# Performance work log

Hardware: AMD Instinct MI355X
Metric: run time of the kernel (lower is better)

## Reference

```python
import jax, jax.numpy as jnp
import numpy as np

B, S, HID = 2, 2048, 1024
NH, NKV = 16, 4
HD = HID // NH          # 64
NREP = NH // NKV        # 4
EPS = 1e-06


def _rotate_half(x):
    h = x.shape[-1] // 2
    return jnp.concatenate([-x[..., h:], x[..., :h]], axis=-1)


def _rope(q, k, cos, sin):
    # q: [b,s,h,d], k: [b,s,kv,d]; cos/sin: [s,d] -> unsqueeze head dim
    c = cos[:, None, :]
    s = sin[:, None, :]
    return q * c + _rotate_half(q) * s, k * c + _rotate_half(k) * s


def setup_inputs() -> dict:
    key = jax.random.key(0)
    ks = jax.random.split(key, 8)
    sc = 0.02
    return {
        "x": jax.random.normal(ks[0], (B, S, HID), jnp.float32),
        "cos": jnp.cos(jnp.arange(S, dtype=jnp.float32)[:, None] *
                       (1.0 / (1e6 ** (jnp.arange(HD, dtype=jnp.float32) / HD)))),
        "sin": jnp.sin(jnp.arange(S, dtype=jnp.float32)[:, None] *
                       (1.0 / (1e6 ** (jnp.arange(HD, dtype=jnp.float32) / HD)))),
        "attention_mask": jnp.ones((B, S), jnp.int32),
        "Wq": jax.random.normal(ks[1], (HID, NH * HD), jnp.float32) * sc,
        "Wk": jax.random.normal(ks[2], (HID, NKV * HD), jnp.float32) * sc,
        "Wv": jax.random.normal(ks[3], (HID, NKV * HD), jnp.float32) * sc,
        "Wo": jax.random.normal(ks[4], (NH * HD, HID), jnp.float32) * sc,
    }


def reference(x, cos, sin, attention_mask, Wq, Wk, Wv, Wo):
    b, s, _ = x.shape
    q = (x @ Wq).reshape(b, s, NH, HD)
    k = (x @ Wk).reshape(b, s, NKV, HD)
    v = (x @ Wv).reshape(b, s, NKV, HD)
    q, k = _rope(q, k, cos[:s], sin[:s])
    # GQA repeat: [b,s,kv,d] -> [b,s,h,d]
    k = jnp.repeat(k, NREP, axis=2)
    v = jnp.repeat(v, NREP, axis=2)
    # -> [b,h,s,d]
    q = jnp.transpose(q, (0, 2, 1, 3))
    k = jnp.transpose(k, (0, 2, 1, 3))
    v = jnp.transpose(v, (0, 2, 1, 3))
    # feature map: elu(x) + 1 (positive features)
    q = jax.nn.elu(q) + 1.0
    k = jax.nn.elu(k) + 1.0
    # prefill path (seq_len > 1): non-causal kernelized scores
    scores = jnp.einsum("bhsd,bhtd->bhst", q, k)  # [b,h,s,s]
    mask = attention_mask[:, None, None, :]       # [b,1,1,s]
    scores = jnp.where(mask == 0, 0.0, scores)
    denom = jnp.clip(
        jax.lax.stop_gradient(jnp.abs(scores).sum(-1, keepdims=True)), 1e-06, None)
    scores = scores / denom
    out = jnp.einsum("bhst,bhtd->bhsd", scores, v)
    out = jnp.transpose(out, (0, 2, 1, 3)).reshape(b, s, NH * HD)
    return out @ Wo
```

## Files before the change

### kernel.cpp

```cpp
#include <hip/hip_runtime.h>
#include <hip/hip_bf16.h>

using u16 = unsigned short;
using u32 = unsigned int;

namespace {
constexpr int S   = 2048;
constexpr int HID = 1024;
constexpr int M   = 4096;
constexpr int K   = 1024;
}

typedef __attribute__((ext_vector_type(8))) short short8;
typedef __attribute__((ext_vector_type(4))) float f32x4;

__device__ __forceinline__ u16 f2bf(float f) {
    u32 u = __builtin_bit_cast(u32, f);
    u += 0x7fffu + ((u >> 16) & 1u);
    return (u16)(u >> 16);
}
__device__ __forceinline__ float bf2f(u16 h) {
    return __builtin_bit_cast(float, (u32)h << 16);
}
__device__ __forceinline__ float phi(float x) {
    return x > 0.f ? x + 1.f : __expf(x);
}
__device__ __forceinline__ void glds16(const u16* g, u16* l) {
    __builtin_amdgcn_global_load_lds(
        (const __attribute__((address_space(1))) u32*)g,
        (__attribute__((address_space(3))) u32*)l, 16, 0, 0);
}

template <int MODE>
__global__ __launch_bounds__(256, 3) void gemm_k(
    const u16* __restrict__ A, const u16* __restrict__ B,
    u16* __restrict__ Cq, float* __restrict__ Ckv,
    float* __restrict__ Cf, int ldc, int zAr, int zBr, int zCr,
    const float* __restrict__ Cos, const float* __restrict__ Sin,
    const int* __restrict__ Mask)
{
    constexpr int BK = 64;
    constexpr int NT = K / BK;
    __shared__ __align__(16) u16 sA0[64 * BK],  sA1[64 * BK];
    __shared__ __align__(16) u16 sB0[128 * BK], sB1[128 * BK];

    A += (size_t)blockIdx.z * zAr * K;
    B += (size_t)blockIdx.z * zBr * K;
    if (MODE == 1) Cf += (size_t)blockIdx.z * zCr * ldc;

    const int tid  = threadIdx.x;
    const int lane = tid & 63, w = tid >> 6;
    const int wm = w & 1, wn = w >> 1;
    const int m0 = blockIdx.x * 64, n0 = blockIdx.y * 128;
    const int fr = lane & 15, fq = lane >> 4;

    const int srow  = lane >> 3;
    const int sslot = lane & 7;
    const int sswz  = (sslot ^ srow) * 8;

    const u16* Asrc = A + (size_t)(m0 + w * 8 + srow) * K + sswz;
    const u16* Bsrc = B + (size_t)(n0 + w * 8 + srow) * K + sswz;
    const int ldsb = (w * 8) * BK;

    f32x4 acc[2][4] = {};

#define STAGE(dA, dB, kt)                                          \
    do {                                                           \
        glds16(Asrc + (kt),                 dA + ldsb);            \
        glds16(Asrc + (size_t)32 * K + (kt), dA + 32 * BK + ldsb); \
        glds16(Bsrc + (kt),                 dB + ldsb);            \
        glds16(Bsrc + (size_t)32 * K + (kt), dB + 32 * BK + ldsb); \
        glds16(Bsrc + (size_t)64 * K + (kt), dB + 64 * BK + ldsb); \
        glds16(Bsrc + (size_t)96 * K + (kt), dB + 96 * BK + ldsb); \
    } while (0)

#define COMPUTE(sAc, sBc)                                                    \
    do {                                                                     \
        _Pragma("unroll")                                                    \
        for (int kk = 0; kk < 2; ++kk) {                                     \
            const int ks = ((kk * 4 + fq) ^ (fr & 7)) * 8;                   \
            short8 ah[2], bh[4];                                             \
            _Pragma("unroll")                                                \
            for (int i = 0; i < 2; ++i)                                      \
                ah[i] = *(const short8*)(sAc + (wm * 32 + i * 16 + fr) * BK + ks); \
            _Pragma("unroll")                                                \
            for (int j = 0; j < 4; ++j)                                      \
                bh[j] = *(const short8*)(sBc + (wn * 64 + j * 16 + fr) * BK + ks); \
            _Pragma("unroll")                                                \
            for (int i = 0; i < 2; ++i)                                      \
                _Pragma("unroll")                                            \
                for (int j = 0; j < 4; ++j)                                  \
                    acc[i][j] = __builtin_amdgcn_mfma_f32_16x16x32_bf16(     \
                        ah[i], bh[j], acc[i][j], 0, 0, 0);                   \
        }                                                                    \
    } while (0)

#define SYNC()                                              \
    do {                                                    \
        asm volatile("s_waitcnt vmcnt(0)" ::: "memory");    \
        __syncthreads();                                    \
    } while (0)

    STAGE(sA0, sB0, 0);
    SYNC();
#pragma unroll 1
    for (int t = 0; t < NT; t += 2) {
        if (t + 1 < NT) STAGE(sA1, sB1, (t + 1) * BK);
        COMPUTE(sA0, sB0);
        SYNC();
        if (t + 2 < NT) STAGE(sA0, sB0, (t + 2) * BK);
        COMPUTE(sA1, sB1);
        SYNC();
    }
#undef STAGE
#undef COMPUTE
#undef SYNC

    const bool isQ = (MODE == 0) && (n0 < 1024);
    const bool isK = (MODE == 0) && (n0 >= 1024) && (n0 < 1280);
#pragma unroll
    for (int i = 0; i < 2; ++i)
#pragma unroll
        for (int jj = 0; jj < 4; ++jj) {
            const int row = m0 + wm * 32 + i * 16 + fq * 4 + jj;
            float v0 = acc[i][0][jj], v1 = acc[i][1][jj];
            float v2 = acc[i][2][jj], v3 = acc[i][3][jj];
            if (MODE == 1) {
                float* cr = &Cf[(size_t)row * ldc + n0 + wn * 64 + fr];
                cr[0] = v0; cr[16] = v1; cr[32] = v2; cr[48] = v3;
                continue;
            }
            if (isQ || isK) {
                const int sb = (row & (S - 1)) * 64;
                float r0 = v0 * Cos[sb + fr]      - v2 * Sin[sb + fr];
                float r2 = v2 * Cos[sb + fr + 32] + v0 * Sin[sb + fr + 32];
                float r1 = v1 * Cos[sb + fr + 16] - v3 * Sin[sb + fr + 16];
                float r3 = v3 * Cos[sb + fr + 48] + v1 * Sin[sb + fr + 48];
                v0 = phi(r0); v1 = phi(r1); v2 = phi(r2); v3 = phi(r3);
            }
            if (isQ) {
                u16* cr = &Cq[(size_t)row * 1024 + n0 + wn * 64 + fr];
                cr[0]  = f2bf(v0); cr[16] = f2bf(v1);
                cr[32] = f2bf(v2); cr[48] = f2bf(v3);
            } else if (isK) {
                const float mv = (float)Mask[row];
                float* cr = &Ckv[(size_t)row * 512 + (n0 - 1024) + wn * 64 + fr];
                cr[0] = v0 * mv; cr[16] = v1 * mv;
                cr[32] = v2 * mv; cr[48] = v3 * mv;
            } else {
                float* cr = &Ckv[(size_t)row * 512 + 256 + (n0 - 1280) + wn * 64 + fr];
                cr[0] = v0; cr[16] = v1; cr[32] = v2; cr[48] = v3;
            }
        }
}

__global__ __launch_bounds__(256) void prep_k(
    const float* __restrict__ X,  u16* __restrict__ Xb,
    const float* __restrict__ Wq, const float* __restrict__ Wk,
    const float* __restrict__ Wv, const float* __restrict__ Wo,
    u16* __restrict__ wt, u16* __restrict__ wot)
{
    const int bid = blockIdx.x, tid = threadIdx.x;
    if (bid < 4096) {
        const int i = (bid * 256 + tid) * 4;
        float4 v = *reinterpret_cast<const float4*>(&X[i]);
        ushort4 h;
        h.x = f2bf(v.x); h.y = f2bf(v.y); h.z = f2bf(v.z); h.w = f2bf(v.w);
        *reinterpret_cast<ushort4*>(&Xb[i]) = h;
        return;
    }
    int r = bid - 4096;
    const float* W; u16* T; int N, nbase, bx, by;
    if (r < 1024)      { W = Wq; T = wt;  N = 1024; nbase = 0;    bx = r & 31; by = r >> 5; }
    else if (r < 1280) { r -= 1024; W = Wk; T = wt; N = 256; nbase = 1024; bx = r & 7; by = r >> 3; }
    else if (r < 1536) { r -= 1280; W = Wv; T = wt; N = 256; nbase = 1280; bx = r & 7; by = r >> 3; }
    else               { r -= 1536; W = Wo; T = wot; N = 1024; nbase = 0;  bx = r & 31; by = r >> 5; }

    __shared__ float t[32][33];
    const int n0 = bx * 32, k0 = by * 32;
    const int tx = tid & 31, ty = tid >> 5;
#pragma unroll
    for (int i = 0; i < 4; ++i)
        t[ty + i * 8][tx] = W[(size_t)(k0 + ty + i * 8) * N + n0 + tx];
    __syncthreads();
#pragma unroll
    for (int i = 0; i < 4; ++i) {
        const int n = ty + i * 8;
        T[(size_t)(nbase + n0 + n) * 1024 + k0 + tx] = f2bf(t[tx][n]);
    }
}

__global__ __launch_bounds__(256) void kv_stage1_k(
    const float* __restrict__ KVf, float* __restrict__ part)
{
    const int g  = blockIdx.x;
    const int ch = blockIdx.y;
    const int b  = g >> 2, kvh = g & 3;
    const int tid = threadIdx.x;

    __shared__ float ks[64][64];
    __shared__ float vs[64][64];
    const int m0 = b * S + ch * 64;
#pragma unroll
    for (int l = 0; l < 4; ++l) {
        int idx = tid + l * 256;
        int r = idx >> 4, q4 = (idx & 15) * 4;
        const float* src = KVf + (size_t)(m0 + r) * 512 + kvh * 64;
        *reinterpret_cast<float4*>(&ks[r][q4]) = *reinterpret_cast<const float4*>(src + q4);
        *reinterpret_cast<float4*>(&vs[r][q4]) = *reinterpret_cast<const float4*>(src + 256 + q4);
    }
    __syncthreads();

    const int i = tid >> 2, j0 = (tid & 3) * 16;
    float4 a0 = {0,0,0,0}, a1 = {0,0,0,0}, a2 = {0,0,0,0}, a3 = {0,0,0,0};
#pragma unroll 8
    for (int r = 0; r < 64; ++r) {
        float kv = ks[r][i];
        float4 w0 = *reinterpret_cast<const float4*>(&vs[r][j0]);
        float4 w1 = *reinterpret_cast<const float4*>(&vs[r][j0 + 4]);
        float4 w2 = *reinterpret_cast<const float4*>(&vs[r][j0 + 8]);
        float4 w3 = *reinterpret_cast<const float4*>(&vs[r][j0 + 12]);
        a0.x = fmaf(kv, w0.x, a0.x); a0.y = fmaf(kv, w0.y, a0.y);
        a0.z = fmaf(kv, w0.z, a0.z); a0.w = fmaf(kv, w0.w, a0.w);
        a1.x = fmaf(kv, w1.x, a1.x); a1.y = fmaf(kv, w1.y, a1.y);
        a1.z = fmaf(kv, w1.z, a1.z); a1.w = fmaf(kv, w1.w, a1.w);
        a2.x = fmaf(kv, w2.x, a2.x); a2.y = fmaf(kv, w2.y, a2.y);
        a2.z = fmaf(kv, w2.z, a2.z); a2.w = fmaf(kv, w2.w, a2.w);
        a3.x = fmaf(kv, w3.x, a3.x); a3.y = fmaf(kv, w3.y, a3.y);
        a3.z = fmaf(kv, w3.z, a3.z); a3.w = fmaf(kv, w3.w, a3.w);
    }
    float* dst = part + ((size_t)g * 32 + ch) * 4160;
    float* d0 = dst + i * 64 + j0;
    *reinterpret_cast<float4*>(d0)      = a0;
    *reinterpret_cast<float4*>(d0 + 4)  = a1;
    *reinterpret_cast<float4*>(d0 + 8)  = a2;
    *reinterpret_cast<float4*>(d0 + 12) = a3;
    if (tid < 64) {
        float ksum = 0.f;
#pragma unroll 8
        for (int r = 0; r < 64; ++r) ksum += ks[r][tid];
        dst[4096 + tid] = ksum;
    }
}

__global__ __launch_bounds__(256) void kv_reduce_k(
    const float* __restrict__ part, u16* __restrict__ KVh,
    float* __restrict__ Ksumf)
{
    const int g = blockIdx.x;
    const int e = blockIdx.y * 256 + threadIdx.x;
    if (e >= 4160) return;
    const float* p = part + (size_t)g * 32 * 4160 + e;
    float s = 0.f;
#pragma unroll 8
    for (int c = 0; c < 32; ++c) s += p[(size_t)c * 4160];
    if (e < 4096) KVh[g * 4096 + e] = f2bf(s);
    else          Ksumf[g * 64 + (e - 4096)] = s;
}

__global__ __launch_bounds__(256, 2) void kw_gemm_k(
    const u16* __restrict__ WoT, const u16* __restrict__ KVb,
    u16* __restrict__ KWT)
{
    __shared__ __align__(16) u16 sA[128 * 64];
    __shared__ __align__(16) u16 sB[64 * 64];

    const int tid = threadIdx.x, lane = tid & 63, w = tid >> 6;
    const int o0 = blockIdx.x * 128;
    const int gh = blockIdx.y, b = gh >> 4, h = gh & 15, g = b * 4 + (h >> 2);
    const int fr = lane & 15, fq = lane >> 4;
    const int srow = lane >> 3, sslot = lane & 7;
    const int sswz = (sslot ^ srow) * 8;

#pragma unroll
    for (int c = 0; c < 4; ++c) {
        const int rb = w * 32 + c * 8;
        glds16(WoT + (size_t)(o0 + rb + srow) * 1024 + h * 64 + sswz, sA + rb * 64);
    }
#pragma unroll
    for (int c = 0; c < 2; ++c) {
        const int rb = w * 16 + c * 8;
        glds16(KVb + (size_t)g * 4096 + (rb + srow) * 64 + sswz, sB + rb * 64);
    }
    asm volatile("s_waitcnt vmcnt(0)" ::: "memory");
    __syncthreads();

    f32x4 acc[2][4] = {};
#pragma unroll
    for (int kk = 0; kk < 2; ++kk) {
        short8 a_h[2], b_h[4];
#pragma unroll
        for (int i = 0; i < 2; ++i) {
            const int row = w * 32 + i * 16 + fr;
            a_h[i] = *(const short8*)(sA + row * 64 + ((kk * 4 + fq) ^ (fr & 7)) * 8);
        }
#pragma unroll
        for (int j = 0; j < 4; ++j) {
            const int row = j * 16 + fr;
            b_h[j] = *(const short8*)(sB + row * 64 + ((kk * 4 + fq) ^ (fr & 7)) * 8);
        }
#pragma unroll
        for (int i = 0; i < 2; ++i)
#pragma unroll
            for (int j = 0; j < 4; ++j)
                acc[i][j] = __builtin_amdgcn_mfma_f32_16x16x32_bf16(
                    a_h[i], b_h[j], acc[i][j], 0, 0, 0);
    }
#pragma unroll
    for (int i = 0; i < 2; ++i)
#pragma unroll
        for (int j = 0; j < 4; ++j)
#pragma unroll
            for (int jj = 0; jj < 4; ++jj) {
                const int row = o0 + w * 32 + i * 16 + fq * 4 + jj;
                const int col = j * 16 + fr;
                KWT[((size_t)b * 1024 + row) * 1024 + h * 64 + col] =
                    f2bf(acc[i][j][jj]);
            }
}

__global__ __launch_bounds__(256) void qhat_k(
    const u16* __restrict__ Qt, const float* __restrict__ Ksumf,
    u16* __restrict__ Qh)
{
    const int t = blockIdx.x * 256 + threadIdx.x;
    const int m = t >> 4, h = t & 15;
    const int g = (m >> 11) * 4 + (h >> 2);
    const u16* q  = Qt + (size_t)m * 1024 + h * 64;
    const float* Ks = Ksumf + g * 64;

    float qv[64];
    float den = 0.f;
#pragma unroll
    for (int c = 0; c < 8; ++c) {
        short8 v8 = *reinterpret_cast<const short8*>(q + c * 8);
#pragma unroll
        for (int j = 0; j < 8; ++j) {
            qv[c * 8 + j] = bf2f((u16)v8[j]);
            den = fmaf(qv[c * 8 + j], Ks[c * 8 + j], den);
        }
    }
    const float rd = 1.f / fmaxf(den, 1e-6f);
    u16* o = Qh + (size_t)m * 1024 + h * 64;
#pragma unroll
    for (int c = 0; c < 8; ++c) {
        short8 ov;
#pragma unroll
        for (int j = 0; j < 8; ++j) ov[j] = (short)f2bf(qv[c * 8 + j] * rd);
        *reinterpret_cast<short8*>(o + c * 8) = ov;
    }
}

extern "C" void kernel_launch(void* const* d_in, const int* in_sizes, int n_in,
                              void* d_out, int out_size, void* d_ws, size_t ws_size,
                              hipStream_t stream)
{
    const float* x    = (const float*)d_in[0];
    const float* cosp = (const float*)d_in[1];
    const float* sinp = (const float*)d_in[2];
    const int*   msk  = (const int*)d_in[3];
    const float* Wq   = (const float*)d_in[4];
    const float* Wk   = (const float*)d_in[5];
    const float* Wv   = (const float*)d_in[6];
    const float* Wo   = (const float*)d_in[7];
    float* out = (float*)d_out;

    u16* xbf  = (u16*)d_ws;
    u16* wt   = xbf  + (size_t)M * K;
    u16* wot  = wt   + (size_t)1536 * K;
    u16* qt   = wot  + (size_t)K * K;
    u16* qhat = qt   + (size_t)M * K;
    u16* kvb  = qhat + (size_t)M * K;
    u16* kwt  = kvb  + 8 * 4096;
    float* kvf   = (float*)(kwt + (size_t)2 * K * K);
    float* part  = kvf + (size_t)M * 512;
    float* ksumf = part + (size_t)8 * 32 * 4160;

    prep_k<<<4096 + 1024 + 256 + 256 + 1024, 256, 0, stream>>>(
        x, xbf, Wq, Wk, Wv, Wo, wt, wot);

    gemm_k<0><<<dim3(M / 64, 1536 / 128, 1), 256, 0, stream>>>(
        xbf, wt, qt, kvf, nullptr, 0, 0, 0, 0, cosp, sinp, msk);

    kv_stage1_k<<<dim3(8, 32), 256, 0, stream>>>(kvf, part);
    kv_reduce_k<<<dim3(8, 17), 256, 0, stream>>>(part, kvb, ksumf);

    kw_gemm_k<<<dim3(8, 32), 256, 0, stream>>>(wot, kvb, kwt);

    qhat_k<<<(M * 16) / 256, 256, 0, stream>>>(qt, ksumf, qhat);

    gemm_k<1><<<dim3(2048 / 64, HID / 128, 2), 256, 0, stream>>>(
        qhat, kwt, nullptr, nullptr, out, HID, 2048, 1024, 2048,
        nullptr, nullptr, nullptr);
}
```

Baseline: 70.14 us.

## Deepen GEMM prefetch pipeline and merge KW gemm with qhat kernel

The GEMM main loop now issues two stages of global-to-LDS loads up front and waits with partial vmcnt counts and raw barriers, so the next tile's loads overlap the current compute instead of draining fully each step. Separately, the KW GEMM and the qhat normalization kernels are merged into one launch, with block index selecting the role, removing a launch and letting both run concurrently. The partial vmcnt count assumes an exact number of outstanding loads per stage, which is fragile. The merged kernel also loses the occupancy hint of 2 in its launch bounds.

```diff
diff --git a/kernel.cpp b/kernel.cpp
--- a/kernel.cpp
+++ b/kernel.cpp
@@ -95,26 +95,27 @@
         }                                                                    \
     } while (0)
 
-#define SYNC()                                              \
-    do {                                                    \
-        asm volatile("s_waitcnt vmcnt(0)" ::: "memory");    \
-        __syncthreads();                                    \
-    } while (0)
-
     STAGE(sA0, sB0, 0);
-    SYNC();
+    STAGE(sA1, sB1, BK);
 #pragma unroll 1
     for (int t = 0; t < NT; t += 2) {
-        if (t + 1 < NT) STAGE(sA1, sB1, (t + 1) * BK);
+        asm volatile("s_waitcnt vmcnt(6)" ::: "memory");
+        __builtin_amdgcn_s_barrier();
         COMPUTE(sA0, sB0);
-        SYNC();
+        asm volatile("s_waitcnt lgkmcnt(0)" ::: "memory");
+        __builtin_amdgcn_s_barrier();
         if (t + 2 < NT) STAGE(sA0, sB0, (t + 2) * BK);
+
+        if (t + 2 < NT) asm volatile("s_waitcnt vmcnt(6)" ::: "memory");
+        else            asm volatile("s_waitcnt vmcnt(0)" ::: "memory");
+        __builtin_amdgcn_s_barrier();
         COMPUTE(sA1, sB1);
-        SYNC();
+        asm volatile("s_waitcnt lgkmcnt(0)" ::: "memory");
+        __builtin_amdgcn_s_barrier();
+        if (t + 3 < NT) STAGE(sA1, sB1, (t + 3) * BK);
     }
 #undef STAGE
 #undef COMPUTE
-#undef SYNC
 
     const bool isQ = (MODE == 0) && (n0 < 1024);
     const bool isK = (MODE == 0) && (n0 >= 1024) && (n0 < 1280);
@@ -258,16 +259,48 @@
     else          Ksumf[g * 64 + (e - 4096)] = s;
 }
 
-__global__ __launch_bounds__(256, 2) void kw_gemm_k(
+__global__ __launch_bounds__(256) void kwqhat_k(
     const u16* __restrict__ WoT, const u16* __restrict__ KVb,
-    u16* __restrict__ KWT)
-{
+    u16* __restrict__ KWT,
+    const u16* __restrict__ Qt, const float* __restrict__ Ksumf,
+    u16* __restrict__ Qh)
+{
+    const int tid = threadIdx.x;
+    if (blockIdx.x >= 256) {
+        const int t = (blockIdx.x - 256) * 256 + tid;
+        const int m = t >> 4, h = t & 15;
+        const int g = (m >> 11) * 4 + (h >> 2);
+        const u16* q  = Qt + (size_t)m * 1024 + h * 64;
+        const float* Ks = Ksumf + g * 64;
+
+        float qv[64];
+        float den = 0.f;
+#pragma unroll
+        for (int c = 0; c < 8; ++c) {
+            short8 v8 = *reinterpret_cast<const short8*>(q + c * 8);
+#pragma unroll
+            for (int j = 0; j < 8; ++j) {
+                qv[c * 8 + j] = bf2f((u16)v8[j]);
+                den = fmaf(qv[c * 8 + j], Ks[c * 8 + j], den);
+            }
+        }
+        const float rd = 1.f / fmaxf(den, 1e-6f);
+        u16* o = Qh + (size_t)m * 1024 + h * 64;
+#pragma unroll
+        for (int c = 0; c < 8; ++c) {
+            short8 ov;
+#pragma unroll
+            for (int j = 0; j < 8; ++j) ov[j] = (short)f2bf(qv[c * 8 + j] * rd);
+            *reinterpret_cast<short8*>(o + c * 8) = ov;
+        }
+        return;
+    }
     __shared__ __align__(16) u16 sA[128 * 64];
     __shared__ __align__(16) u16 sB[64 * 64];
 
-    const int tid = threadIdx.x, lane = tid & 63, w = tid >> 6;
-    const int o0 = blockIdx.x * 128;
-    const int gh = blockIdx.y, b = gh >> 4, h = gh & 15, g = b * 4 + (h >> 2);
+    const int lane = tid & 63, w = tid >> 6;
+    const int o0 = (blockIdx.x & 7) * 128;
+    const int gh = blockIdx.x >> 3, b = gh >> 4, h = gh & 15, g = b * 4 + (h >> 2);
     const int fr = lane & 15, fq = lane >> 4;
     const int srow = lane >> 3, sslot = lane & 7;
     const int sswz = (sslot ^ srow) * 8;
@@ -317,38 +350,6 @@
                 KWT[((size_t)b * 1024 + row) * 1024 + h * 64 + col] =
                     f2bf(acc[i][j][jj]);
             }
-}
-
-__global__ __launch_bounds__(256) void qhat_k(
-    const u16* __restrict__ Qt, const float* __restrict__ Ksumf,
-    u16* __restrict__ Qh)
-{
-    const int t = blockIdx.x * 256 + threadIdx.x;
-    const int m = t >> 4, h = t & 15;
-    const int g = (m >> 11) * 4 + (h >> 2);
-    const u16* q  = Qt + (size_t)m * 1024 + h * 64;
-    const float* Ks = Ksumf + g * 64;
-
-    float qv[64];
-    float den = 0.f;
-#pragma unroll
-    for (int c = 0; c < 8; ++c) {
-        short8 v8 = *reinterpret_cast<const short8*>(q + c * 8);
-#pragma unroll
-        for (int j = 0; j < 8; ++j) {
-            qv[c * 8 + j] = bf2f((u16)v8[j]);
-            den = fmaf(qv[c * 8 + j], Ks[c * 8 + j], den);
-        }
-    }
-    const float rd = 1.f / fmaxf(den, 1e-6f);
-    u16* o = Qh + (size_t)m * 1024 + h * 64;
-#pragma unroll
-    for (int c = 0; c < 8; ++c) {
-        short8 ov;
-#pragma unroll
-        for (int j = 0; j < 8; ++j) ov[j] = (short)f2bf(qv[c * 8 + j] * rd);
-        *reinterpret_cast<short8*>(o + c * 8) = ov;
-    }
 }
 
 extern "C" void kernel_launch(void* const* d_in, const int* in_sizes, int n_in,
@@ -385,9 +386,7 @@
     kv_stage1_k<<<dim3(8, 32), 256, 0, stream>>>(kvf, part);
     kv_reduce_k<<<dim3(8, 17), 256, 0, stream>>>(part, kvb, ksumf);
 
-    kw_gemm_k<<<dim3(8, 32), 256, 0, stream>>>(wot, kvb, kwt);
-
-    qhat_k<<<(M * 16) / 256, 256, 0, stream>>>(qt, ksumf, qhat);
+    kwqhat_k<<<512, 256, 0, stream>>>(wot, kvb, kwt, qt, ksumf, qhat);
 
     gemm_k<1><<<dim3(2048 / 64, HID / 128, 2), 256, 0, stream>>>(
         qhat, kwt, nullptr, nullptr, out, HID, 2048, 1024, 2048,
```

After: 70.22 us. About the same (+0.1%).
